# Optimization experiments

Hardware: AMD Instinct MI355X
Metric: run time of the kernel (lower is better)

## Reference

```python
import jax, jax.numpy as jnp
import numpy as np

NSUB = 4  # fixed RK4 substeps per observation interval (stand-in for adaptive dopri5)


def _gru(x_t, h, Wih, Whh, bih, bhh):
    # torch.nn.GRUCell math
    gi = x_t @ Wih.T + bih          # [B, 3H]
    gh = h @ Whh.T + bhh            # [B, 3H]
    gi_r, gi_z, gi_n = jnp.split(gi, 3, axis=-1)
    gh_r, gh_z, gh_n = jnp.split(gh, 3, axis=-1)
    r = jax.nn.sigmoid(gi_r + gh_r)
    z = jax.nn.sigmoid(gi_z + gh_z)
    n = jnp.tanh(gi_n + r * gh_n)
    return (1.0 - z) * n + z * h


def _ode_f(h, W1, b1, W2, b2):
    # ODEFunc(hidden_dim): Linear -> tanh -> Linear (autonomous)
    return jnp.tanh(h @ W1.T + b1) @ W2.T + b2


def setup_inputs() -> dict:
    B, T, I, H, L = 1024, 128, 128, 512, 64
    key = jax.random.key(0)
    ks = jax.random.split(key, 10)
    init = lambda k, shape, fan: (jax.random.normal(k, shape, jnp.float32) / np.sqrt(fan)).astype(jnp.float32)
    return {
        "x": jax.random.normal(ks[0], (B, T, I), jnp.float32),
        "t": jnp.arange(T, dtype=jnp.float32) * 0.1,  # increasing observation times
        "Wih": init(ks[1], (3 * H, I), I),
        "Whh": init(ks[2], (3 * H, H), H),
        "bih": jnp.zeros((3 * H,), jnp.float32),
        "bhh": jnp.zeros((3 * H,), jnp.float32),
        "W1": init(ks[3], (H, H), H),
        "b1": jnp.zeros((H,), jnp.float32),
        "W2": init(ks[4], (H, H), H),
        "b2": jnp.zeros((H,), jnp.float32),
        "Wmu": init(ks[5], (L, H), H),
        "bmu": jnp.zeros((L,), jnp.float32),
        "Wlv": init(ks[6], (L, H), H),
        "blv": jnp.zeros((L,), jnp.float32),
    }


def reference(x, t, Wih, Whh, bih, bhh, W1, b1, W2, b2, Wmu, bmu, Wlv, blv):
    B = x.shape[0]
    H = Whh.shape[1]
    f = lambda h: _ode_f(h, W1, b1, W2, b2)

    def rk4_evolve(h, dt):
        hs = dt / NSUB
        for _ in range(NSUB):
            k1 = f(h)
            k2 = f(h + 0.5 * hs * k1)
            k3 = f(h + 0.5 * hs * k2)
            k4 = f(h + hs * k3)
            h = h + (hs / 6.0) * (k1 + 2.0 * k2 + 2.0 * k3 + k4)
        return h

    h0 = _gru(x[:, 0, :], jnp.zeros((B, H), x.dtype), Wih, Whh, bih, bhh)
    xs = (jnp.swapaxes(x[:, 1:, :], 0, 1), t[1:] - t[:-1])  # ([T-1,B,I], [T-1])

    def step(h, inp):
        xi, dt = inp
        h = rk4_evolve(h, dt)
        h = _gru(xi, h, Wih, Whh, bih, bhh)
        return h, None

    hT, _ = jax.lax.scan(step, h0, xs)
    mu = hT @ Wmu.T + bmu
    logvar = hT @ Wlv.T + blv
    return mu, logvar
```

## Files before the change

kernel.cpp:

```cpp
#include <hip/hip_runtime.h>
#include <stdint.h>

typedef __bf16 bf16;
typedef __bf16 bf16x8 __attribute__((ext_vector_type(8)));
typedef __bf16 bf16x4 __attribute__((ext_vector_type(4)));
typedef float f32x4 __attribute__((ext_vector_type(4)));

__global__ void pack_split(const float* __restrict__ src, bf16* __restrict__ dst,
                           int N, int K, int NFtot, int nfBase)
{
    int gid = blockIdx.x * 256 + threadIdx.x;
    if (gid >= N * K) return;
    int n = gid / K, k = gid - n * K;
    int KS = K >> 5;
    float x = src[gid];
    bf16 hb = (bf16)x;
    bf16 lb = (bf16)(x - (float)hb);
    int nf = nfBase + (n >> 4);
    int l  = (n & 15) | (((k & 31) >> 3) << 4);
    int ks = k >> 5;
    int e  = k & 7;
    int base = ((nf * KS + ks) << 9) + (l << 3) + e;
    int half = NFtot * KS * 512;
    dst[base] = hb;
    dst[half + base] = lb;
}

#define MFMA(a, b, c) __builtin_amdgcn_mfma_f32_16x16x32_bf16(a, b, c, 0, 0, 0)

template<int NFR, int KS, int NFtot, int STRIDE>
__device__ __forceinline__ void mm_stream(const bf16* __restrict__ pk, int nf0, int lane,
                                          const bf16* __restrict__ S, f32x4* acc)
{
    const int halfoff = NFtot * KS * 512;
#pragma unroll
    for (int i = 0; i < NFR; ++i) { f32x4 z = {0.f, 0.f, 0.f, 0.f}; acc[i] = z; }
#pragma unroll 2
    for (int ks = 0; ks < KS; ++ks) {
        bf16x8 ah = *(const bf16x8*)(S + ((ks << 6) + lane) * 8);
        bf16x8 al = *(const bf16x8*)(S + 8192 + ((ks << 6) + lane) * 8);
#pragma unroll
        for (int i = 0; i < NFR; ++i) {
            int nf = (i >> 1) * STRIDE + nf0 + (i & 1);
            const bf16* pb = pk + ((nf * KS + ks) << 9) + (lane << 3);
            bf16x8 bh = *(const bf16x8*)pb;
            bf16x8 bl = *(const bf16x8*)(pb + halfoff);
            acc[i] = MFMA(ah, bh, acc[i]);
            acc[i] = MFMA(al, bh, acc[i]);
            acc[i] = MFMA(ah, bl, acc[i]);
        }
    }
}

template<int NFR, int KS>
__device__ __forceinline__ void mm_stream2(const bf16* __restrict__ pk, int nf0, int lane,
                                           const bf16* __restrict__ S, f32x4* acc)
{
#pragma unroll
    for (int i = 0; i < NFR; ++i) { f32x4 z = {0.f, 0.f, 0.f, 0.f}; acc[i] = z; }
#pragma unroll 2
    for (int ks = 0; ks < KS; ++ks) {
        bf16x8 ah = *(const bf16x8*)(S + ((ks << 6) + lane) * 8);
        bf16x8 al = *(const bf16x8*)(S + 8192 + ((ks << 6) + lane) * 8);
#pragma unroll
        for (int i = 0; i < NFR; ++i) {
            const bf16* pb = pk + (((nf0 + i) * KS + ks) << 9) + (lane << 3);
            bf16x8 bh = *(const bf16x8*)pb;
            acc[i] = MFMA(ah, bh, acc[i]);
            acc[i] = MFMA(al, bh, acc[i]);
        }
    }
}

template<int NFR, int NFtot, int STRIDE>
__device__ __forceinline__ void mm_x(const bf16* __restrict__ pk, int nf0, int lane,
                                     const bf16x8* xh, const bf16x8* xl, f32x4* acc)
{
    const int KS = 4;
    const int halfoff = NFtot * KS * 512;
#pragma unroll
    for (int i = 0; i < NFR; ++i) { f32x4 z = {0.f, 0.f, 0.f, 0.f}; acc[i] = z; }
#pragma unroll
    for (int ks = 0; ks < 4; ++ks)
#pragma unroll
        for (int i = 0; i < NFR; ++i) {
            int nf = (i >> 1) * STRIDE + nf0 + (i & 1);
            const bf16* pb = pk + ((nf * KS + ks) << 9) + (lane << 3);
            bf16x8 bh = *(const bf16x8*)pb;
            bf16x8 bl = *(const bf16x8*)(pb + halfoff);
            acc[i] = MFMA(xh[ks], bh, acc[i]);
            acc[i] = MFMA(xl[ks], bh, acc[i]);
            acc[i] = MFMA(xh[ks], bl, acc[i]);
        }
}

__device__ __forceinline__ void scat(bf16* __restrict__ Sp, int r, int c, float v)
{
    bf16 hb = (bf16)v;
    bf16 lb = (bf16)(v - (float)hb);
    int off = (((c >> 5) << 6) + (r | (((c & 31) >> 3) << 4))) * 8 + (c & 7);
    Sp[off] = hb;
    Sp[8192 + off] = lb;
}

__global__ __launch_bounds__(1024, 4)
void odegru_persist(const float* __restrict__ x, const float* __restrict__ t,
                    const float* __restrict__ bih, const float* __restrict__ bhh,
                    const float* __restrict__ b1,  const float* __restrict__ b2,
                    const float* __restrict__ bmu, const float* __restrict__ blv,
                    const bf16* __restrict__ pkW1, const bf16* __restrict__ pkW2,
                    const bf16* __restrict__ pkWhh, const bf16* __restrict__ pkWih,
                    const bf16* __restrict__ pkWout, float* __restrict__ out)
{
    __shared__ float hbuf[16 * 512];
    __shared__ bf16  S[2 * 16 * 64 * 8];

    const int tid  = threadIdx.x;
    const int lane = tid & 63;
    const int w    = tid >> 6;
    const int li   = lane & 15, lh = lane >> 4;
    const int m0   = blockIdx.x << 4;
    const int Tn = 128, In = 128;

    const int c0 = (w << 5) + li;
    const int rb = lh << 2;

    float b1c[2], b2c[2], bihr[2], bihz[2], bihn[2], bhhr[2], bhhz[2], bhhn[2];
#pragma unroll
    for (int fi = 0; fi < 2; ++fi) {
        int c = c0 + (fi << 4);
        b1c[fi] = b1[c];  b2c[fi] = b2[c];
        bihr[fi] = bih[c]; bihz[fi] = bih[512 + c]; bihn[fi] = bih[1024 + c];
        bhhr[fi] = bhh[c]; bhhz[fi] = bhh[512 + c]; bhhn[fi] = bhh[1024 + c];
    }

    f32x4 acc[2];
    float ksum[2][4];
    f32x4 giacc[6], ghacc[6];

    const int Ho = 8 * 16 * 512;

    for (int s = 0; s < 128; ++s) {
        const float dt = (s > 0) ? (t[s] - t[s - 1]) : 0.f;
        if (s > 0) {
            const float a01 = dt * 0.125f, a2 = dt * 0.25f, hk = dt * (1.f / 24.f);
#pragma unroll 1
            for (int sub = 0; sub < 4; ++sub) {
#pragma unroll 1
                for (int st = 0; st < 4; ++st) {
                    mm_stream2<2, 16>(pkW1, w << 1, lane, S, acc);
                    __syncthreads();
#pragma unroll
                    for (int fi = 0; fi < 2; ++fi)
#pragma unroll
                        for (int rg = 0; rg < 4; ++rg)
                            scat(S, rb + rg, c0 + (fi << 4), tanhf(acc[fi][rg] + b1c[fi]));
                    __syncthreads();
                    mm_stream2<2, 16>(pkW2, w << 1, lane, S, acc);
                    __syncthreads();
                    const float al = (st < 2) ? a01 : a2;
#pragma unroll
                    for (int fi = 0; fi < 2; ++fi)
#pragma unroll
                        for (int rg = 0; rg < 4; ++rg) {
                            float v = acc[fi][rg] + b2c[fi];
                            int c = c0 + (fi << 4);
                            int hoff = (rb + rg) * 512 + c;
                            if (st == 0) ksum[fi][rg] = v;
                            else if (st < 3) ksum[fi][rg] += 2.f * v;
                            float nv;
                            if (st < 3) {
                                nv = hbuf[hoff] + al * v;
                            } else {
                                nv = hbuf[hoff] + hk * (ksum[fi][rg] + v);
                                hbuf[hoff] = nv;
                            }
                            scat(S, rb + rg, c, nv);
                        }
                    __syncthreads();
                }
            }
        }
        bf16x8 xh[4], xl[4];
        {
            const float* xp = x + ((long)(m0 + li) * Tn + s) * In + (lh << 3);
#pragma unroll
            for (int ks = 0; ks < 4; ++ks) {
                f32x4 v0 = *(const f32x4*)(xp + (ks << 5));
                f32x4 v1 = *(const f32x4*)(xp + (ks << 5) + 4);
                bf16x8 h8, l8;
#pragma unroll
                for (int j = 0; j < 4; ++j) {
                    bf16 hb = (bf16)v0[j]; h8[j] = hb;     l8[j] = (bf16)(v0[j] - (float)hb);
                    bf16 h2 = (bf16)v1[j]; h8[4 + j] = h2; l8[4 + j] = (bf16)(v1[j] - (float)h2);
                }
                xh[ks] = h8; xl[ks] = l8;
            }
        }
        mm_x<6, 96, 32>(pkWih, w << 1, lane, xh, xl, giacc);
        if (s > 0) {
            mm_stream<6, 16, 96, 32>(pkWhh, w << 1, lane, S, ghacc);
        } else {
#pragma unroll
            for (int i = 0; i < 6; ++i) { f32x4 z = {0.f, 0.f, 0.f, 0.f}; ghacc[i] = z; }
        }
        __syncthreads();
#pragma unroll
        for (int fi = 0; fi < 2; ++fi)
#pragma unroll
            for (int rg = 0; rg < 4; ++rg) {
                int c = c0 + (fi << 4);
                int hoff = (rb + rg) * 512 + c;
                float gr = giacc[fi][rg] + bihr[fi] + ghacc[fi][rg] + bhhr[fi];
                float gz = giacc[2 + fi][rg] + bihz[fi] + ghacc[2 + fi][rg] + bhhz[fi];
                float rr = 1.f / (1.f + __expf(-gr));
                float zz = 1.f / (1.f + __expf(-gz));
                float nn = tanhf(giacc[4 + fi][rg] + bihn[fi] + rr * (ghacc[4 + fi][rg] + bhhn[fi]));
                float hold = (s > 0) ? hbuf[hoff] : 0.f;
                float hn = (1.f - zz) * nn + zz * hold;
                hbuf[hoff] = hn;
                scat(S, rb + rg, c, hn);
            }
        __syncthreads();
    }
    if (w < 8) {
        f32x4 oacc[1];
        mm_stream<1, 16, 8, 0>(pkWout, w, lane, S, oacc);
        const float* bo = (w < 4) ? bmu : blv;
        int cl = ((w & 3) << 4) + li;
        float bv = bo[cl];
        float* ob = out + ((w < 4) ? 0 : 65536);
#pragma unroll
        for (int rg = 0; rg < 4; ++rg)
            ob[(long)(m0 + rb + rg) * 64 + cl] = oacc[0][rg] + bv;
    }
}

extern "C" void kernel_launch(void* const* d_in, const int* in_sizes, int n_in,
                              void* d_out, int out_size, void* d_ws, size_t ws_size,
                              hipStream_t stream)
{
    (void)in_sizes; (void)n_in; (void)out_size; (void)ws_size;
    const float* x   = (const float*)d_in[0];
    const float* t   = (const float*)d_in[1];
    const float* Wih = (const float*)d_in[2];
    const float* Whh = (const float*)d_in[3];
    const float* bih = (const float*)d_in[4];
    const float* bhh = (const float*)d_in[5];
    const float* W1  = (const float*)d_in[6];
    const float* b1  = (const float*)d_in[7];
    const float* W2  = (const float*)d_in[8];
    const float* b2  = (const float*)d_in[9];
    const float* Wmu = (const float*)d_in[10];
    const float* bmu = (const float*)d_in[11];
    const float* Wlv = (const float*)d_in[12];
    const float* blv = (const float*)d_in[13];
    float* out = (float*)d_out;

    bf16* pk1  = (bf16*)d_ws;
    bf16* pk2  = pk1 + 524288;
    bf16* pkhh = pk2 + 524288;
    bf16* pkih = pkhh + 1572864;
    bf16* pkout = pkih + 393216;

    pack_split<<<1024, 256, 0, stream>>>(W1,  pk1,  512, 512, 32, 0);
    pack_split<<<1024, 256, 0, stream>>>(W2,  pk2,  512, 512, 32, 0);
    pack_split<<<3072, 256, 0, stream>>>(Whh, pkhh, 1536, 512, 96, 0);
    pack_split<<<768,  256, 0, stream>>>(Wih, pkih, 1536, 128, 96, 0);
    pack_split<<<128,  256, 0, stream>>>(Wmu, pkout, 64, 512, 8, 0);
    pack_split<<<128,  256, 0, stream>>>(Wlv, pkout, 64, 512, 8, 4);

    odegru_persist<<<64, 1024, 0, stream>>>(x, t, bih, bhh, b1, b2, bmu, blv,
                                            pk1, pk2, pkhh, pkih, pkout, out);
}
```

Baseline: 29.04 ms.

## Prefetch ODE weight fragments into registers and keep hidden state in registers

Replaces the ODE matmul loop with a fully unrolled version that keeps a six-deep ring of W1/W2 fragments in registers, so global/L2 weight loads are issued ahead of the MFMAs that use them. The fp32 hidden state moves from a shared-memory buffer into per-thread registers, since each thread only ever touches its own 8 elements, removing the LDS reads and writes in the RK4 and GRU updates. The occupancy hint becomes amdgpu_waves_per_eu(4,4). The cost is higher register pressure, which could cause spills under the fixed occupancy target.

```diff
diff --git a/kernel.cpp b/kernel.cpp
--- a/kernel.cpp
+++ b/kernel.cpp
@@ -3,7 +3,6 @@
 
 typedef __bf16 bf16;
 typedef __bf16 bf16x8 __attribute__((ext_vector_type(8)));
-typedef __bf16 bf16x4 __attribute__((ext_vector_type(4)));
 typedef float f32x4 __attribute__((ext_vector_type(4)));
 
 __global__ void pack_split(const float* __restrict__ src, bf16* __restrict__ dst,
@@ -28,6 +27,36 @@
 
 #define MFMA(a, b, c) __builtin_amdgcn_mfma_f32_16x16x32_bf16(a, b, c, 0, 0, 0)
 
+template<int KS, int DEPTH>
+__device__ __forceinline__ void mm_stream2p(const bf16* __restrict__ pk, int nf0, int lane,
+                                            const bf16* __restrict__ S, f32x4* acc)
+{
+    const bf16* pb0 = pk + ((nf0 * KS) << 9) + (lane << 3);
+    const bf16* pb1 = pk + (((nf0 + 1) * KS) << 9) + (lane << 3);
+    bf16x8 b0[DEPTH], b1[DEPTH];
+#pragma unroll
+    for (int p = 0; p < DEPTH; ++p) {
+        b0[p] = *(const bf16x8*)(pb0 + (p << 9));
+        b1[p] = *(const bf16x8*)(pb1 + (p << 9));
+    }
+    f32x4 z = {0.f, 0.f, 0.f, 0.f};
+    acc[0] = z; acc[1] = z;
+#pragma unroll
+    for (int ks = 0; ks < KS; ++ks) {
+        const int sl = ks % DEPTH;
+        bf16x8 ah = *(const bf16x8*)(S + ((ks << 6) + lane) * 8);
+        bf16x8 al = *(const bf16x8*)(S + 8192 + ((ks << 6) + lane) * 8);
+        acc[0] = MFMA(ah, b0[sl], acc[0]);
+        acc[0] = MFMA(al, b0[sl], acc[0]);
+        acc[1] = MFMA(ah, b1[sl], acc[1]);
+        acc[1] = MFMA(al, b1[sl], acc[1]);
+        if (ks + DEPTH < KS) {
+            b0[sl] = *(const bf16x8*)(pb0 + ((ks + DEPTH) << 9));
+            b1[sl] = *(const bf16x8*)(pb1 + ((ks + DEPTH) << 9));
+        }
+    }
+}
+
 template<int NFR, int KS, int NFtot, int STRIDE>
 __device__ __forceinline__ void mm_stream(const bf16* __restrict__ pk, int nf0, int lane,
                                           const bf16* __restrict__ S, f32x4* acc)
@@ -52,26 +81,6 @@
     }
 }
 
-template<int NFR, int KS>
-__device__ __forceinline__ void mm_stream2(const bf16* __restrict__ pk, int nf0, int lane,
-                                           const bf16* __restrict__ S, f32x4* acc)
-{
-#pragma unroll
-    for (int i = 0; i < NFR; ++i) { f32x4 z = {0.f, 0.f, 0.f, 0.f}; acc[i] = z; }
-#pragma unroll 2
-    for (int ks = 0; ks < KS; ++ks) {
-        bf16x8 ah = *(const bf16x8*)(S + ((ks << 6) + lane) * 8);
-        bf16x8 al = *(const bf16x8*)(S + 8192 + ((ks << 6) + lane) * 8);
-#pragma unroll
-        for (int i = 0; i < NFR; ++i) {
-            const bf16* pb = pk + (((nf0 + i) * KS + ks) << 9) + (lane << 3);
-            bf16x8 bh = *(const bf16x8*)pb;
-            acc[i] = MFMA(ah, bh, acc[i]);
-            acc[i] = MFMA(al, bh, acc[i]);
-        }
-    }
-}
-
 template<int NFR, int NFtot, int STRIDE>
 __device__ __forceinline__ void mm_x(const bf16* __restrict__ pk, int nf0, int lane,
                                      const bf16x8* xh, const bf16x8* xl, f32x4* acc)
@@ -103,7 +112,7 @@
     Sp[8192 + off] = lb;
 }
 
-__global__ __launch_bounds__(1024, 4)
+__global__ __attribute__((amdgpu_waves_per_eu(4, 4))) __launch_bounds__(1024)
 void odegru_persist(const float* __restrict__ x, const float* __restrict__ t,
                     const float* __restrict__ bih, const float* __restrict__ bhh,
                     const float* __restrict__ b1,  const float* __restrict__ b2,
@@ -112,8 +121,7 @@
                     const bf16* __restrict__ pkWhh, const bf16* __restrict__ pkWih,
                     const bf16* __restrict__ pkWout, float* __restrict__ out)
 {
-    __shared__ float hbuf[16 * 512];
-    __shared__ bf16  S[2 * 16 * 64 * 8];
+    __shared__ bf16 S[2 * 16 * 64 * 8];
 
     const int tid  = threadIdx.x;
     const int lane = tid & 63;
@@ -136,6 +144,7 @@
 
     f32x4 acc[2];
     float ksum[2][4];
+    float h8[2][4];
     f32x4 giacc[6], ghacc[6];
 
     const int Ho = 8 * 16 * 512;
@@ -148,7 +157,7 @@
             for (int sub = 0; sub < 4; ++sub) {
 #pragma unroll 1
                 for (int st = 0; st < 4; ++st) {
-                    mm_stream2<2, 16>(pkW1, w << 1, lane, S, acc);
+                    mm_stream2p<16, 6>(pkW1, w << 1, lane, S, acc);
                     __syncthreads();
 #pragma unroll
                     for (int fi = 0; fi < 2; ++fi)
@@ -156,7 +165,7 @@
                         for (int rg = 0; rg < 4; ++rg)
                             scat(S, rb + rg, c0 + (fi << 4), tanhf(acc[fi][rg] + b1c[fi]));
                     __syncthreads();
-                    mm_stream2<2, 16>(pkW2, w << 1, lane, S, acc);
+                    mm_stream2p<16, 6>(pkW2, w << 1, lane, S, acc);
                     __syncthreads();
                     const float al = (st < 2) ? a01 : a2;
 #pragma unroll
@@ -165,15 +174,14 @@
                         for (int rg = 0; rg < 4; ++rg) {
                             float v = acc[fi][rg] + b2c[fi];
                             int c = c0 + (fi << 4);
-                            int hoff = (rb + rg) * 512 + c;
                             if (st == 0) ksum[fi][rg] = v;
                             else if (st < 3) ksum[fi][rg] += 2.f * v;
                             float nv;
                             if (st < 3) {
-                                nv = hbuf[hoff] + al * v;
+                                nv = h8[fi][rg] + al * v;
                             } else {
-                                nv = hbuf[hoff] + hk * (ksum[fi][rg] + v);
-                                hbuf[hoff] = nv;
+                                nv = h8[fi][rg] + hk * (ksum[fi][rg] + v);
+                                h8[fi][rg] = nv;
                             }
                             scat(S, rb + rg, c, nv);
                         }
@@ -188,13 +196,13 @@
             for (int ks = 0; ks < 4; ++ks) {
                 f32x4 v0 = *(const f32x4*)(xp + (ks << 5));
                 f32x4 v1 = *(const f32x4*)(xp + (ks << 5) + 4);
-                bf16x8 h8, l8;
+                bf16x8 h8v, l8v;
 #pragma unroll
                 for (int j = 0; j < 4; ++j) {
-                    bf16 hb = (bf16)v0[j]; h8[j] = hb;     l8[j] = (bf16)(v0[j] - (float)hb);
-                    bf16 h2 = (bf16)v1[j]; h8[4 + j] = h2; l8[4 + j] = (bf16)(v1[j] - (float)h2);
+                    bf16 hb = (bf16)v0[j]; h8v[j] = hb;     l8v[j] = (bf16)(v0[j] - (float)hb);
+                    bf16 h2 = (bf16)v1[j]; h8v[4 + j] = h2; l8v[4 + j] = (bf16)(v1[j] - (float)h2);
                 }
-                xh[ks] = h8; xl[ks] = l8;
+                xh[ks] = h8v; xl[ks] = l8v;
             }
         }
         mm_x<6, 96, 32>(pkWih, w << 1, lane, xh, xl, giacc);
@@ -210,15 +218,14 @@
 #pragma unroll
             for (int rg = 0; rg < 4; ++rg) {
                 int c = c0 + (fi << 4);
-                int hoff = (rb + rg) * 512 + c;
                 float gr = giacc[fi][rg] + bihr[fi] + ghacc[fi][rg] + bhhr[fi];
                 float gz = giacc[2 + fi][rg] + bihz[fi] + ghacc[2 + fi][rg] + bhhz[fi];
                 float rr = 1.f / (1.f + __expf(-gr));
                 float zz = 1.f / (1.f + __expf(-gz));
                 float nn = tanhf(giacc[4 + fi][rg] + bihn[fi] + rr * (ghacc[4 + fi][rg] + bhhn[fi]));
-                float hold = (s > 0) ? hbuf[hoff] : 0.f;
+                float hold = (s > 0) ? h8[fi][rg] : 0.f;
                 float hn = (1.f - zz) * nn + zz * hold;
-                hbuf[hoff] = hn;
+                h8[fi][rg] = hn;
                 scat(S, rb + rg, c, hn);
             }
         __syncthreads();
```

Result: slower. 66.33 ms (+128.4%).
